# Kernel tuning notes

Hardware: AMD Instinct MI355X
Metric: run time of the kernel (lower is better)

The kernel has to match this reference:

```python
import jax, jax.numpy as jnp
import numpy as np

H = 16          # query heads
HKV = 4         # kv heads
DK = 128        # head_qk_dim
DV = 128        # head_v_dim
HID = 2048
KSZ = 4         # conv kernel size
EPS = 1e-5
NORMALIZER = 16.0


def _causal_dwconv_silu(x, w):
    # x: (B,S,C), w: (C,K). Causal depthwise conv then SiLU.
    B, S, C = x.shape
    K = w.shape[1]
    xp = jnp.pad(x, ((0, 0), (K - 1, 0), (0, 0)))
    y = jnp.zeros_like(x)
    for i in range(K):  # K=4, tiny fixed loop
        y = y + w[:, i] * xp[:, i:i + S, :]
    return jax.nn.silu(y)


def _l2norm(x, eps=1e-6):
    return x * jax.lax.rsqrt(jnp.sum(x * x, axis=-1, keepdims=True) + eps)


def setup_inputs() -> dict:
    key = jax.random.key(0)
    ks = jax.random.split(key, 8)
    B, S = 2, 2048
    qkv_dim = H * DK + HKV * DK + HKV * DV  # 3072
    s = lambda fan_in: 1.0 / np.sqrt(fan_in)
    return {
        "hidden_states": jax.random.normal(ks[0], (B, S, HID), jnp.float32),
        "qkv_w": jax.random.uniform(ks[1], (qkv_dim, HID), jnp.float32, -s(HID), s(HID)),
        "g_w": jax.random.uniform(ks[2], (H * DV, HID), jnp.float32, -s(HID), s(HID)),
        "b_w": jax.random.uniform(ks[3], (H, HID), jnp.float32, -s(HID), s(HID)),
        "gk_w": jax.random.uniform(ks[4], (H, HID), jnp.float32, -s(HID), s(HID)),
        "conv_w": jax.random.uniform(ks[5], (qkv_dim, KSZ), jnp.float32, -s(KSZ), s(KSZ)),
        "out_norm_w": jnp.ones((DV,), jnp.float32),
        "o_w": jax.random.uniform(ks[6], (HID, H * DV), jnp.float32, -s(H * DV), s(H * DV)),
    }


def reference(hidden_states, qkv_w, g_w, b_w, gk_w, conv_w, out_norm_w, o_w):
    x = hidden_states
    B, S, _ = x.shape
    grp = H // HKV

    qkv = x @ qkv_w.T                                   # (B,S,3072)
    qkv = _causal_dwconv_silu(qkv, conv_w)
    q, k, v = jnp.split(qkv, [H * DK, H * DK + HKV * DK], axis=-1)
    q = q.reshape(B, S, H, DK)
    k = k.reshape(B, S, HKV, DK)
    v = v.reshape(B, S, HKV, DV)
    # GQA expansion
    k = jnp.repeat(k, grp, axis=2)                      # (B,S,H,DK)
    v = jnp.repeat(v, grp, axis=2)                      # (B,S,H,DV)

    # q/k L2 norm + scale
    q = _l2norm(q) * (DK ** -0.5)
    k = _l2norm(k)

    # decay gate (logsigmoid, log-space), write strength beta
    g_log = jax.nn.log_sigmoid(x @ gk_w.T) / NORMALIZER  # (B,S,H)
    alpha = jnp.exp(g_log)
    beta = jax.nn.sigmoid(x @ b_w.T)                     # (B,S,H)

    # gated delta rule: S_t = a_t*S_{t-1} + k_t (x) beta_t*(v_t - k_t @ (a_t*S_{t-1}))
    def step(Sstate, inp):
        q_t, k_t, v_t, a_t, b_t = inp                    # (B,H,*)
        Sstate = Sstate * a_t[..., None, None]           # (B,H,DK,DV)
        v_pred = jnp.einsum('bhk,bhkv->bhv', k_t, Sstate)
        delta = (v_t - v_pred) * b_t[..., None]
        Sstate = Sstate + jnp.einsum('bhk,bhv->bhkv', k_t, delta)
        o_t = jnp.einsum('bhk,bhkv->bhv', q_t, Sstate)
        return Sstate, o_t

    tfirst = lambda a: jnp.moveaxis(a, 1, 0)             # (S,B,H,...)
    S0 = jnp.zeros((B, H, DK, DV), x.dtype)
    _, o = jax.lax.scan(step, S0, (tfirst(q), tfirst(k), tfirst(v), tfirst(alpha), tfirst(beta)))
    o = jnp.moveaxis(o, 0, 1)                            # (B,S,H,DV)

    # gated per-head RMSNorm then output projection
    g = (x @ g_w.T).reshape(B, S, H, DV)
    o = o * jax.lax.rsqrt(jnp.mean(o * o, axis=-1, keepdims=True) + EPS) * out_norm_w
    o = o * jax.nn.silu(g)
    return (o.reshape(B, S, H * DV)) @ o_w.T
```

## Files before the change

kernel.cpp:

```cpp
#include <hip/hip_runtime.h>
#include <math.h>

#define S_LEN 2048
#define BATCH 2
#define NH 16
#define NKV 4
#define DKQ 128
#define DVV 128
#define HID 2048
#define QKV_DIM 3072
#define M_TOK 4096

typedef _Float16 halfx8 __attribute__((ext_vector_type(8)));
typedef _Float16 halfx4 __attribute__((ext_vector_type(4)));
typedef float floatx4 __attribute__((ext_vector_type(4)));

#define AS1 __attribute__((address_space(1)))
#define AS3 __attribute__((address_space(3)))
#define GLD16(gp, lp) __builtin_amdgcn_global_load_lds((AS1 const void*)(gp), (AS3 void*)(lp), 16, 0, 0)
#define MFMA16(a, b, c) __builtin_amdgcn_mfma_f32_16x16x32_f16(a, b, c, 0, 0, 0)
#define SBAR() asm volatile("s_barrier" ::: "memory")

#define PA_STRIDE 81920

__device__ __forceinline__ float sigmoidf_(float x) { return 1.f / (1.f + __expf(-x)); }

__global__ __launch_bounds__(256) void cvt_f16(const float* __restrict__ in,
                                               _Float16* __restrict__ out, int n8) {
  int i = blockIdx.x * 256 + threadIdx.x;
  if (i >= n8) return;
  const float4* p = (const float4*)in;
  float4 a = p[2 * (size_t)i], b = p[2 * (size_t)i + 1];
  halfx8 o;
  o[0] = (_Float16)a.x; o[1] = (_Float16)a.y; o[2] = (_Float16)a.z; o[3] = (_Float16)a.w;
  o[4] = (_Float16)b.x; o[5] = (_Float16)b.y; o[6] = (_Float16)b.z; o[7] = (_Float16)b.w;
  *(halfx8*)(out + (size_t)i * 8) = o;
}

__global__ __launch_bounds__(256, 2) void gemm_bt_f16_2ph(const _Float16* __restrict__ A,
                                                          const _Float16* __restrict__ B,
                                                          float* __restrict__ C,
                                                          int M, int N, int K) {
  __shared__ char lds[65536] __attribute__((aligned(16)));
  const int tid = threadIdx.x;
  const int wid = tid >> 6, l = tid & 63;
  const int lr = l & 15, hi = l >> 4;
  const int wm = wid & 1, wn = wid >> 1;

  int nbx = gridDim.x;
  int bid = blockIdx.y * nbx + blockIdx.x;
  int nwg = nbx * gridDim.y;
  int swz = (nwg & 7) ? bid : ((bid & 7) * (nwg >> 3) + (bid >> 3));
  int bm = (swz / nbx) * 128, bn = (swz % nbx) * 128;

  const int srow = tid >> 3;
  const int csrc = ((tid & 7) ^ ((tid >> 3) & 7)) * 8;
  const _Float16* ga[4];
  const _Float16* gb[4];
#pragma unroll
  for (int q = 0; q < 4; ++q) {
    ga[q] = A + (size_t)(bm + q * 32 + srow) * K + csrc;
    gb[q] = B + (size_t)(bn + q * 32 + srow) * K + csrc;
  }
  const int dstA = tid * 16;
  const int dstB = 16384 + tid * 16;

  int cr[2];
  cr[0] = (hi ^ (lr & 7)) * 16;
  cr[1] = ((4 + hi) ^ (lr & 7)) * 16;
  const int abase = wm * 8192 + lr * 128;
  const int bbase = 16384 + wn * 8192 + lr * 128;

  floatx4 acc[4][4];
#pragma unroll
  for (int i = 0; i < 4; ++i)
#pragma unroll
    for (int j = 0; j < 4; ++j) acc[i][j] = (floatx4){0.f, 0.f, 0.f, 0.f};

  const int NT = K >> 6;
#define STAGE8(tt, pp)                                           \
  {                                                              \
    int kof = (tt) * 64;                                         \
    int pof = (pp) * 32768;                                      \
    _Pragma("unroll") for (int q = 0; q < 4; ++q) {              \
      GLD16(ga[q] + kof, lds + pof + q * 4096 + dstA);           \
      GLD16(gb[q] + kof, lds + pof + q * 4096 + dstB);           \
    }                                                            \
  }

  STAGE8(0, 0);
  asm volatile("s_waitcnt vmcnt(0)" ::: "memory");
  SBAR();

  halfx8 af[4][2], bf[2][2];
  for (int t = 0; t < NT; ++t) {
    const char* bufc = lds + (t & 1) * 32768;
    if (t + 1 < NT) STAGE8(t + 1, (t + 1) & 1);
#pragma unroll
    for (int mi = 0; mi < 4; ++mi)
#pragma unroll
      for (int ks = 0; ks < 2; ++ks)
        af[mi][ks] = *(const halfx8*)(bufc + abase + mi * 2048 + cr[ks]);
#pragma unroll
    for (int ni = 0; ni < 2; ++ni)
#pragma unroll
      for (int ks = 0; ks < 2; ++ks)
        bf[ni][ks] = *(const halfx8*)(bufc + bbase + ni * 2048 + cr[ks]);
    SBAR();
    __builtin_amdgcn_s_setprio(1);
#pragma unroll
    for (int mi = 0; mi < 4; ++mi)
#pragma unroll
      for (int ni = 0; ni < 2; ++ni)
#pragma unroll
        for (int ks = 0; ks < 2; ++ks)
          acc[mi][ni] = MFMA16(af[mi][ks], bf[ni][ks], acc[mi][ni]);
    __builtin_amdgcn_s_setprio(0);
    SBAR();
#pragma unroll
    for (int ni = 0; ni < 2; ++ni)
#pragma unroll
      for (int ks = 0; ks < 2; ++ks)
        bf[ni][ks] = *(const halfx8*)(bufc + bbase + (ni + 2) * 2048 + cr[ks]);
    SBAR();
    __builtin_amdgcn_s_setprio(1);
#pragma unroll
    for (int mi = 0; mi < 4; ++mi)
#pragma unroll
      for (int ni = 0; ni < 2; ++ni)
#pragma unroll
        for (int ks = 0; ks < 2; ++ks)
          acc[mi][ni + 2] = MFMA16(af[mi][ks], bf[ni][ks], acc[mi][ni + 2]);
    __builtin_amdgcn_s_setprio(0);
    asm volatile("s_waitcnt vmcnt(0)" ::: "memory");
    SBAR();
  }
#pragma unroll
  for (int mi = 0; mi < 4; ++mi)
#pragma unroll
    for (int ni = 0; ni < 4; ++ni) {
      int row0 = bm + wm * 64 + mi * 16 + hi * 4;
      int col = bn + wn * 64 + ni * 16 + lr;
#pragma unroll
      for (int r = 0; r < 4; ++r)
        C[(size_t)(row0 + r) * N + col] = acc[mi][ni][r];
    }
#undef STAGE8
}

__global__ __launch_bounds__(256) void gkb_kernel(const float* __restrict__ X,
                                                  const float* __restrict__ gk_w,
                                                  const float* __restrict__ b_w,
                                                  float* __restrict__ glog,
                                                  float* __restrict__ be) {
  __shared__ float xs[16][260];
  __shared__ float ws[32][260];
  int tid = threadIdx.x;
  int m0 = blockIdx.x * 16;
  int tl = tid >> 4, n0 = tid & 15;
  float acc0 = 0.f, acc1 = 0.f;
  for (int k0 = 0; k0 < HID; k0 += 256) {
#pragma unroll
    for (int i = 0; i < 4; ++i) {
      int F = i * 256 + tid;
      int r = F >> 6, c4 = (F & 63) * 4;
      *(float4*)&xs[r][c4] = *(const float4*)&X[(size_t)(m0 + r) * HID + k0 + c4];
    }
#pragma unroll
    for (int i = 0; i < 8; ++i) {
      int F = i * 256 + tid;
      int r = F >> 6, c4 = (F & 63) * 4;
      const float* src = (r < 16) ? (gk_w + (size_t)r * HID) : (b_w + (size_t)(r - 16) * HID);
      *(float4*)&ws[r][c4] = *(const float4*)&src[k0 + c4];
    }
    __syncthreads();
#pragma unroll 16
    for (int k = 0; k < 256; k += 4) {
      float4 a = *(const float4*)&xs[tl][k];
      float4 w0 = *(const float4*)&ws[n0][k];
      float4 w1 = *(const float4*)&ws[n0 + 16][k];
      acc0 += a.x * w0.x + a.y * w0.y + a.z * w0.z + a.w * w0.w;
      acc1 += a.x * w1.x + a.y * w1.y + a.z * w1.z + a.w * w1.w;
    }
    __syncthreads();
  }
  int m = m0 + tl, b = m >> 11, s = m & (S_LEN - 1);
  float z = acc0;
  float ls = (z >= 0.f) ? -log1pf(expf(-z)) : (z - log1pf(expf(z)));
  size_t oi = (size_t)(b * NH + n0) * S_LEN + s;
  glog[oi] = ls * 0.0625f;
  be[oi] = sigmoidf_(acc1);
}

__global__ __launch_bounds__(256) void conv_kernel(const float* __restrict__ qkv,
                                                   const float* __restrict__ conv_w,
                                                   float* __restrict__ qn,
                                                   float* __restrict__ kn,
                                                   float* __restrict__ vn) {
  __shared__ float ys[QKV_DIM];
  __shared__ float sc[20];
  int m = blockIdx.x;
  int b = m >> 11, s = m & (S_LEN - 1);
  int tid = threadIdx.x;
  for (int c = tid; c < QKV_DIM; c += 256) {
    float acc = 0.f;
#pragma unroll
    for (int i = 0; i < 4; ++i) {
      int si = s - 3 + i;
      if (si >= 0) acc += conv_w[c * 4 + i] * qkv[(size_t)(b * S_LEN + si) * QKV_DIM + c];
    }
    ys[c] = acc * (1.f / (1.f + __expf(-acc)));
  }
  __syncthreads();
  int wv = tid >> 6, lane = tid & 63;
  for (int ch = wv; ch < 20; ch += 4) {
    int base = (ch < 16) ? ch * 128 : 2048 + (ch - 16) * 128;
    float x0 = ys[base + lane], x1 = ys[base + 64 + lane];
    float ss = x0 * x0 + x1 * x1;
#pragma unroll
    for (int off = 1; off < 64; off <<= 1) ss += __shfl_xor(ss, off);
    float scale = rsqrtf(ss + 1e-6f);
    if (ch < 16) scale *= 0.08838834764831845f;
    if (lane == 0) sc[ch] = scale;
  }
  __syncthreads();
  for (int c = tid; c < 2048; c += 256) {
    int h = c >> 7, d = c & 127;
    qn[((size_t)(b * NH + h) * S_LEN + s) * DKQ + d] = ys[c] * sc[h];
  }
  for (int c = tid; c < 512; c += 256) {
    int j = c >> 7, d = c & 127;
    kn[((size_t)(b * NKV + j) * S_LEN + s) * DKQ + d] = ys[2048 + c] * sc[16 + j];
    vn[((size_t)(b * NKV + j) * S_LEN + s) * DVV + d] = ys[2560 + c];
  }
}

__global__ __launch_bounds__(256, 2) void phaseA_kernel(const float* __restrict__ qn,
                                                        const float* __restrict__ kn,
                                                        const float* __restrict__ vn,
                                                        const float* __restrict__ glog,
                                                        const float* __restrict__ be,
                                                        char* __restrict__ pout,
                                                        float* __restrict__ obuf) {
  __shared__ char smem[80128] __attribute__((aligned(16)));
  _Float16* kh = (_Float16*)smem;
  _Float16* qh = (_Float16*)(smem + 22528);
  float*    LT = (float*)(smem + 45056);
  _Float16* Ph = (_Float16*)(smem + 67584);
  float*    sc_c    = (float*)(smem + 78848);
  float*    sc_beta = sc_c + 64;
  float*    sc_gam  = sc_c + 128;
  float*    sc_bg   = sc_c + 192;
  float*    sc_gcr  = sc_c + 256;
  _Float16* Dt = (_Float16*)smem;
  _Float16* Wt = (_Float16*)(smem + 22528);
  _Float16* Kt = (_Float16*)(smem + 45056);

  int u = blockIdx.x;
  int bh = u >> 5, ch = u & 31;
  int t0 = ch * 64;
  int b = bh >> 4, h = bh & 15, kvh = h >> 2;
  const float* qb = qn + ((size_t)bh * S_LEN + t0) * DKQ;
  const float* kb = kn + (((size_t)(b * NKV + kvh)) * S_LEN + t0) * DKQ;
  const float* vb = vn + (((size_t)(b * NKV + kvh)) * S_LEN + t0) * DVV;
  const float* gl = glog + (size_t)bh * S_LEN + t0;
  const float* ber = be + (size_t)bh * S_LEN + t0;
  char* base = pout + (size_t)u * PA_STRIDE;
  _Float16* M_out = (_Float16*)base;
  _Float16* E_out = (_Float16*)(base + 32768);
  _Float16* B_out = (_Float16*)(base + 49152);
  float* ob = obuf + ((size_t)bh * S_LEN + t0) * DVV;

  int tid = threadIdx.x;
  if (tid < 64) {
    float x = gl[tid];
#pragma unroll
    for (int off = 1; off < 64; off <<= 1) {
      float y = __shfl_up(x, off);
      if (tid >= off) x += y;
    }
    sc_c[tid] = x;
  }
#pragma unroll
  for (int i = 0; i < 8; ++i) {
    int idx = i * 256 + tid;
    int t = idx >> 5, d4 = (idx & 31) * 4;
    float4 kv4 = *(const float4*)&kb[(size_t)t * DKQ + d4];
    float4 qv4 = *(const float4*)&qb[(size_t)t * DKQ + d4];
    _Float16* kd = &kh[t * 152 + d4];
    kd[0] = (_Float16)kv4.x; kd[1] = (_Float16)kv4.y; kd[2] = (_Float16)kv4.z; kd[3] = (_Float16)kv4.w;
    _Float16* qd = &qh[t * 152 + d4];
    qd[0] = (_Float16)qv4.x; qd[1] = (_Float16)qv4.y; qd[2] = (_Float16)qv4.z; qd[3] = (_Float16)qv4.w;
  }
  __syncthreads();
  if (tid < 64) {
    float c = sc_c[tid], c63 = sc_c[63];
    float gam = __expf(c);
    float bet = ber[tid];
    sc_gam[tid] = gam; sc_beta[tid] = bet; sc_bg[tid] = bet * gam;
    sc_gcr[tid] = __expf(c63 - c);
  }
  __syncthreads();

  float z[64];
  {
    const float* src = (tid < 128) ? vb : kb;
    const float* mult = (tid < 128) ? sc_beta : sc_bg;
    int col = tid & 127;
#pragma unroll
    for (int t = 0; t < 64; ++t) z[t] = mult[t] * src[(size_t)t * 128 + col];
  }

  int w = tid >> 6, l = tid & 63;
  int lr = l & 15, lk8 = (l >> 4) * 8, q4 = (l >> 4) * 4;
  floatx4 acc[8];
#pragma unroll
  for (int i = 0; i < 8; ++i) acc[i] = (floatx4){0.f, 0.f, 0.f, 0.f};
#pragma unroll
  for (int job = 0; job < 8; ++job) {
    int j2 = w * 8 + job;
    int tm = (j2 & 15) >> 2, tn = j2 & 3;
    const _Float16* Ar = (j2 < 16) ? kh : qh;
#pragma unroll
    for (int kk = 0; kk < 4; ++kk) {
      halfx8 af = *(const halfx8*)&Ar[(tm * 16 + lr) * 152 + kk * 32 + lk8];
      halfx8 bf = *(const halfx8*)&kh[(tn * 16 + lr) * 152 + kk * 32 + lk8];
      acc[job] = MFMA16(af, bf, acc[job]);
    }
  }
#pragma unroll
  for (int job = 0; job < 8; ++job) {
    int j2 = w * 8 + job;
    int tm = (j2 & 15) >> 2, tn = j2 & 3;
    int jcol = tn * 16 + lr;
    float cj = sc_c[jcol];
#pragma unroll
    for (int r = 0; r < 4; ++r) {
      int trow = tm * 16 + q4 + r;
      float val = acc[job][r] * __expf(sc_c[trow] - cj);
      if (j2 < 16) {
        LT[jcol * 68 + trow] = (jcol < trow) ? sc_beta[trow] * val : 0.f;
      } else {
        Ph[trow * 88 + jcol] = (_Float16)((jcol <= trow) ? val : 0.f);
      }
    }
  }
  __syncthreads();

#pragma unroll
  for (int t = 0; t < 64; ++t) {
    float zt = z[t];
    const int start = ((t + 1) >> 2) << 2;
#pragma unroll
    for (int t2 = start; t2 < 64; t2 += 4) {
      float4 lv = *(const float4*)&LT[t * 68 + t2];
      z[t2 + 0] -= lv.x * zt;
      z[t2 + 1] -= lv.y * zt;
      z[t2 + 2] -= lv.z * zt;
      z[t2 + 3] -= lv.w * zt;
    }
  }
  floatx4 Eacc[8];
#pragma unroll
  for (int ni = 0; ni < 8; ++ni)
#pragma unroll
    for (int r = 0; r < 4; ++r) {
      int trow = w * 16 + q4 + r;
      Eacc[ni][r] = sc_gam[trow] * (float)qh[trow * 152 + ni * 16 + lr];
    }
  __syncthreads();

  {
    int d = tid >> 1, tb = (tid & 1) * 32;
#pragma unroll
    for (int j = 0; j < 4; ++j) {
      halfx8 kv;
#pragma unroll
      for (int r = 0; r < 8; ++r) {
        int t = tb + j * 8 + r;
        kv[r] = (_Float16)(sc_gcr[t] * (float)kh[t * 152 + d]);
      }
      *(halfx8*)&Kt[d * 88 + tb + j * 8] = kv;
    }
  }
  if (tid >= 128) {
    int col = tid & 127;
#pragma unroll
    for (int t = 0; t < 64; t += 8) {
      halfx8 wv;
#pragma unroll
      for (int r = 0; r < 8; ++r) wv[r] = (_Float16)(-z[t + r]);
      *(halfx8*)&Wt[col * 88 + t] = wv;
    }
  }
  __syncthreads();
  if (tid < 128) {
    int col = tid & 127;
#pragma unroll
    for (int t = 0; t < 64; t += 8) {
      halfx8 dv;
#pragma unroll
      for (int r = 0; r < 8; ++r) dv[r] = (_Float16)z[t + r];
      *(halfx8*)&Dt[col * 88 + t] = dv;
    }
  }
  __syncthreads();

  floatx4 Macc[2][8], Bacc[2][8], Oacc[8];
  float gC = __expf(sc_c[63]);
#pragma unroll
  for (int mi = 0; mi < 2; ++mi)
#pragma unroll
    for (int ni = 0; ni < 8; ++ni) {
#pragma unroll
      for (int r = 0; r < 4; ++r)
        Macc[mi][ni][r] = ((w * 32 + mi * 16 + q4 + r) == (ni * 16 + lr)) ? gC : 0.f;
      Bacc[mi][ni] = (floatx4){0.f, 0.f, 0.f, 0.f};
    }
#pragma unroll
  for (int ni = 0; ni < 8; ++ni) Oacc[ni] = (floatx4){0.f, 0.f, 0.f, 0.f};
#pragma unroll
  for (int ks = 0; ks < 2; ++ks) {
    halfx8 ka0 = *(const halfx8*)&Kt[(w * 32 + lr) * 88 + ks * 32 + lk8];
    halfx8 ka1 = *(const halfx8*)&Kt[(w * 32 + 16 + lr) * 88 + ks * 32 + lk8];
    halfx8 pa = *(const halfx8*)&Ph[(w * 16 + lr) * 88 + ks * 32 + lk8];
#pragma unroll
    for (int ni = 0; ni < 8; ++ni) {
      halfx8 wb = *(const halfx8*)&Wt[(ni * 16 + lr) * 88 + ks * 32 + lk8];
      halfx8 db = *(const halfx8*)&Dt[(ni * 16 + lr) * 88 + ks * 32 + lk8];
      Macc[0][ni] = MFMA16(ka0, wb, Macc[0][ni]);
      Macc[1][ni] = MFMA16(ka1, wb, Macc[1][ni]);
      Bacc[0][ni] = MFMA16(ka0, db, Bacc[0][ni]);
      Bacc[1][ni] = MFMA16(ka1, db, Bacc[1][ni]);
      Eacc[ni] = MFMA16(pa, wb, Eacc[ni]);
      Oacc[ni] = MFMA16(pa, db, Oacc[ni]);
    }
  }
#pragma unroll
  for (int mi = 0; mi < 2; ++mi)
#pragma unroll
    for (int ni = 0; ni < 8; ++ni)
#pragma unroll
      for (int r = 0; r < 4; ++r) {
        int row = w * 32 + mi * 16 + q4 + r;
        M_out[row * 128 + ni * 16 + lr] = (_Float16)Macc[mi][ni][r];
        B_out[ni * 2048 + row * 16 + lr] = (_Float16)Bacc[mi][ni][r];
      }
#pragma unroll
  for (int ni = 0; ni < 8; ++ni)
#pragma unroll
    for (int r = 0; r < 4; ++r) {
      int trow = w * 16 + q4 + r;
      E_out[trow * 128 + ni * 16 + lr] = (_Float16)Eacc[ni][r];
      ob[(size_t)trow * 128 + ni * 16 + lr] = Oacc[ni][r];
    }
}

__global__ __launch_bounds__(256, 1) void phaseB_kernel(const char* __restrict__ pin,
                                                        float* __restrict__ obuf) {
  __shared__ _Float16 Mh[2][128 * 152];
  __shared__ _Float16 Eh[2][64 * 152];
  __shared__ _Float16 St[2][16 * 152];

  int bh = blockIdx.x & 31, vg = blockIdx.x >> 5;
  int tid = threadIdx.x, w = tid >> 6, l = tid & 63;
  int lr = l & 15, lk8 = (l >> 4) * 8, q4 = (l >> 4) * 4;
  const char* ub0 = pin + (size_t)(bh * 32) * PA_STRIDE;
  float* ob_base = obuf + (size_t)bh * S_LEN * DVV + vg * 16;

  float4 Mr[8], Er[4];
  float Bc[2][4], Oc[4], Bn[2][4], On[4];

  {
    const float4* Mg = (const float4*)ub0;
    const float4* Eg = (const float4*)(ub0 + 32768);
    const _Float16* Bg = (const _Float16*)(ub0 + 49152) + vg * 2048;
#pragma unroll
    for (int j = 0; j < 8; ++j) Mr[j] = Mg[j * 256 + tid];
#pragma unroll
    for (int j = 0; j < 4; ++j) Er[j] = Eg[j * 256 + tid];
#pragma unroll
    for (int mi = 0; mi < 2; ++mi)
#pragma unroll
      for (int r = 0; r < 4; ++r)
        Bc[mi][r] = (float)Bg[(w * 32 + mi * 16 + q4 + r) * 16 + lr];
#pragma unroll
    for (int r = 0; r < 4; ++r)
      Oc[r] = ob_base[(size_t)(w * 16 + q4 + r) * DVV + lr];
#pragma unroll
    for (int j = 0; j < 8; ++j) {
      int n = j * 256 + tid;
      *(float4*)&Mh[0][(n >> 4) * 152 + (n & 15) * 8] = Mr[j];
    }
#pragma unroll
    for (int j = 0; j < 4; ++j) {
      int n = j * 256 + tid;
      *(float4*)&Eh[0][(n >> 4) * 152 + (n & 15) * 8] = Er[j];
    }
    halfx4 z4;
    z4[0] = (_Float16)0.f; z4[1] = (_Float16)0.f; z4[2] = (_Float16)0.f; z4[3] = (_Float16)0.f;
#pragma unroll
    for (int mi = 0; mi < 2; ++mi)
      *(halfx4*)&St[0][lr * 152 + w * 32 + mi * 16 + q4] = z4;
  }
  asm volatile("s_waitcnt lgkmcnt(0)" ::: "memory");

  for (int c = 0; c < 32; ++c) {
    __builtin_amdgcn_s_barrier();
    int cur = c & 1, nxt = cur ^ 1;
    bool have = (c + 1) < 32;
    if (have) {
      const char* un = ub0 + (size_t)(c + 1) * PA_STRIDE;
      const float4* Mg = (const float4*)un;
      const float4* Eg = (const float4*)(un + 32768);
      const _Float16* Bg = (const _Float16*)(un + 49152) + vg * 2048;
#pragma unroll
      for (int j = 0; j < 8; ++j) Mr[j] = Mg[j * 256 + tid];
#pragma unroll
      for (int j = 0; j < 4; ++j) Er[j] = Eg[j * 256 + tid];
#pragma unroll
      for (int mi = 0; mi < 2; ++mi)
#pragma unroll
        for (int r = 0; r < 4; ++r)
          Bn[mi][r] = (float)Bg[(w * 32 + mi * 16 + q4 + r) * 16 + lr];
#pragma unroll
      for (int r = 0; r < 4; ++r)
        On[r] = ob_base[(size_t)((c + 1) * 64 + w * 16 + q4 + r) * DVV + lr];
    }
    floatx4 Sn0 = {Bc[0][0], Bc[0][1], Bc[0][2], Bc[0][3]};
    floatx4 Sn1 = {Bc[1][0], Bc[1][1], Bc[1][2], Bc[1][3]};
    floatx4 Oa = {Oc[0], Oc[1], Oc[2], Oc[3]};
#pragma unroll
    for (int ks = 0; ks < 4; ++ks) {
      halfx8 sf = *(const halfx8*)&St[cur][lr * 152 + ks * 32 + lk8];
      halfx8 ma0 = *(const halfx8*)&Mh[cur][(w * 32 + lr) * 152 + ks * 32 + lk8];
      halfx8 ma1 = *(const halfx8*)&Mh[cur][(w * 32 + 16 + lr) * 152 + ks * 32 + lk8];
      halfx8 ea = *(const halfx8*)&Eh[cur][(w * 16 + lr) * 152 + ks * 32 + lk8];
      Sn0 = MFMA16(ma0, sf, Sn0);
      Sn1 = MFMA16(ma1, sf, Sn1);
      Oa = MFMA16(ea, sf, Oa);
    }
    {
      float* obr = ob_base + (size_t)c * 64 * DVV;
#pragma unroll
      for (int r = 0; r < 4; ++r)
        obr[(size_t)(w * 16 + q4 + r) * DVV + lr] = Oa[r];
    }
#pragma unroll
    for (int mi = 0; mi < 2; ++mi) {
      halfx4 sv;
      floatx4 Sm = mi ? Sn1 : Sn0;
#pragma unroll
      for (int r = 0; r < 4; ++r) sv[r] = (_Float16)Sm[r];
      *(halfx4*)&St[nxt][lr * 152 + w * 32 + mi * 16 + q4] = sv;
    }
    if (have) {
#pragma unroll
      for (int j = 0; j < 8; ++j) {
        int n = j * 256 + tid;
        *(float4*)&Mh[nxt][(n >> 4) * 152 + (n & 15) * 8] = Mr[j];
      }
#pragma unroll
      for (int j = 0; j < 4; ++j) {
        int n = j * 256 + tid;
        *(float4*)&Eh[nxt][(n >> 4) * 152 + (n & 15) * 8] = Er[j];
      }
#pragma unroll
      for (int mi = 0; mi < 2; ++mi)
#pragma unroll
        for (int r = 0; r < 4; ++r) Bc[mi][r] = Bn[mi][r];
#pragma unroll
      for (int r = 0; r < 4; ++r) Oc[r] = On[r];
    }
    asm volatile("s_waitcnt lgkmcnt(0)" ::: "memory");
  }
}

__global__ __launch_bounds__(256) void normgate_kernel(const float* __restrict__ o_buf,
                                                       const float* __restrict__ g_buf,
                                                       const float* __restrict__ nw,
                                                       _Float16* __restrict__ og) {
  int gid = blockIdx.x * 4 + (threadIdx.x >> 6);
  int lane = threadIdx.x & 63;
  int m = gid >> 4, h = gid & 15;
  int b = m >> 11, s = m & (S_LEN - 1);
  const float* orow = o_buf + ((size_t)(b * NH + h) * S_LEN + s) * DVV;
  float o0 = orow[lane], o1 = orow[lane + 64];
  float ss = o0 * o0 + o1 * o1;
#pragma unroll
  for (int off = 1; off < 64; off <<= 1) ss += __shfl_xor(ss, off);
  float r = rsqrtf(ss * (1.f / 128.f) + 1e-5f);
  size_t gi = (size_t)m * HID + h * DVV;
  float g0 = g_buf[gi + lane], g1 = g_buf[gi + lane + 64];
  og[gi + lane] = (_Float16)(o0 * r * nw[lane] * (g0 * sigmoidf_(g0)));
  og[gi + lane + 64] = (_Float16)(o1 * r * nw[lane + 64] * (g1 * sigmoidf_(g1)));
}

extern "C" void kernel_launch(void* const* d_in, const int* in_sizes, int n_in,
                              void* d_out, int out_size, void* d_ws, size_t ws_size,
                              hipStream_t stream) {
  const float* X      = (const float*)d_in[0];
  const float* qkv_w  = (const float*)d_in[1];
  const float* g_w    = (const float*)d_in[2];
  const float* b_w    = (const float*)d_in[3];
  const float* gk_w   = (const float*)d_in[4];
  const float* conv_w = (const float*)d_in[5];
  const float* norm_w = (const float*)d_in[6];
  const float* o_w    = (const float*)d_in[7];
  float* out = (float*)d_out;

  char* ws = (char*)d_ws;
  float* qkv_buf   = (float*)(ws);
  float* g_buf     = (float*)(ws);
  _Float16* ow16   = (_Float16*)(ws + 33554432);
  float* glog      = (float*)(ws + 41943040);
  float* be        = (float*)(ws + 42205184);
  float* qn        = (float*)(ws + 50331648);
  float* kn        = (float*)(ws + 83886080);
  float* vn        = (float*)(ws + 92274688);
  _Float16* X16    = (_Float16*)(ws + 100663296);
  _Float16* qw16   = (_Float16*)(ws + 117440512);
  _Float16* gw16   = (_Float16*)(ws + 130023424);
  char*  pA        = (char*)(ws + 100663296);
  _Float16* og16   = (_Float16*)(ws + 100663296);
  float* o_buf     = qn;

  dim3 blk(256);
  cvt_f16<<<dim3(4096), blk, 0, stream>>>(X, X16, 1048576);
  cvt_f16<<<dim3(3072), blk, 0, stream>>>(qkv_w, qw16, 786432);
  cvt_f16<<<dim3(2048), blk, 0, stream>>>(g_w, gw16, 524288);
  gemm_bt_f16_2ph<<<dim3(QKV_DIM / 128, M_TOK / 128), blk, 0, stream>>>(X16, qw16, qkv_buf, M_TOK, QKV_DIM, HID);
  conv_kernel<<<dim3(M_TOK), blk, 0, stream>>>(qkv_buf, conv_w, qn, kn, vn);
  gkb_kernel<<<dim3(M_TOK / 16), blk, 0, stream>>>(X, gk_w, b_w, glog, be);
  cvt_f16<<<dim3(2048), blk, 0, stream>>>(o_w, ow16, 524288);
  gemm_bt_f16_2ph<<<dim3(HID / 128, M_TOK / 128), blk, 0, stream>>>(X16, gw16, g_buf, M_TOK, HID, HID);
  phaseA_kernel<<<dim3(1024), blk, 0, stream>>>(qn, kn, vn, glog, be, pA, o_buf);
  phaseB_kernel<<<dim3(256), blk, 0, stream>>>(pA, o_buf);
  normgate_kernel<<<dim3(M_TOK * NH / 4), blk, 0, stream>>>(o_buf, g_buf, norm_w, og16);
  gemm_bt_f16_2ph<<<dim3(HID / 128, M_TOK / 128), blk, 0, stream>>>(og16, ow16, out, M_TOK, HID, HID);
}
```

Baseline: 487.8 us.

## Restructure conv kernel to slide a register window over 8 tokens per wave

The causal depthwise conv kernel now gives each wave 8 consecutive tokens of one 128-channel head slot. It keeps the previous three inputs in registers as a sliding window, so each qkv element is read from global memory once per wave instead of four times. The per-head L2 norm becomes a wave shuffle reduction with no shared memory or block barriers. The grid changes from one block per token to a 2D tile×slot launch, and the conv weights are loaded once as float4 per thread.

```diff
diff --git a/kernel.cpp b/kernel.cpp
--- a/kernel.cpp
+++ b/kernel.cpp
@@ -197,41 +197,52 @@
                                                    float* __restrict__ qn,
                                                    float* __restrict__ kn,
                                                    float* __restrict__ vn) {
-  __shared__ float ys[QKV_DIM];
-  __shared__ float sc[20];
-  int m = blockIdx.x;
-  int b = m >> 11, s = m & (S_LEN - 1);
-  int tid = threadIdx.x;
-  for (int c = tid; c < QKV_DIM; c += 256) {
-    float acc = 0.f;
-#pragma unroll
-    for (int i = 0; i < 4; ++i) {
-      int si = s - 3 + i;
-      if (si >= 0) acc += conv_w[c * 4 + i] * qkv[(size_t)(b * S_LEN + si) * QKV_DIM + c];
-    }
-    ys[c] = acc * (1.f / (1.f + __expf(-acc)));
-  }
-  __syncthreads();
-  int wv = tid >> 6, lane = tid & 63;
-  for (int ch = wv; ch < 20; ch += 4) {
-    int base = (ch < 16) ? ch * 128 : 2048 + (ch - 16) * 128;
-    float x0 = ys[base + lane], x1 = ys[base + 64 + lane];
-    float ss = x0 * x0 + x1 * x1;
-#pragma unroll
-    for (int off = 1; off < 64; off <<= 1) ss += __shfl_xor(ss, off);
-    float scale = rsqrtf(ss + 1e-6f);
-    if (ch < 16) scale *= 0.08838834764831845f;
-    if (lane == 0) sc[ch] = scale;
-  }
-  __syncthreads();
-  for (int c = tid; c < 2048; c += 256) {
-    int h = c >> 7, d = c & 127;
-    qn[((size_t)(b * NH + h) * S_LEN + s) * DKQ + d] = ys[c] * sc[h];
-  }
-  for (int c = tid; c < 512; c += 256) {
-    int j = c >> 7, d = c & 127;
-    kn[((size_t)(b * NKV + j) * S_LEN + s) * DKQ + d] = ys[2048 + c] * sc[16 + j];
-    vn[((size_t)(b * NKV + j) * S_LEN + s) * DVV + d] = ys[2560 + c];
+  int tile = blockIdx.x, slot = blockIdx.y;
+  int w = threadIdx.x >> 6, l = threadIdx.x & 63;
+  int m0 = tile * 32 + w * 8;
+  int b = m0 >> 11, s0 = m0 & (S_LEN - 1);
+  int cbase = (slot < 16) ? slot * 128 : (slot < 20 ? 2048 + (slot - 16) * 128
+                                                    : 2560 + (slot - 20) * 128);
+  int c0 = cbase + l, c1 = c0 + 64;
+  float4 wv0 = *(const float4*)&conv_w[c0 * 4];
+  float4 wv1 = *(const float4*)&conv_w[c1 * 4];
+
+  float a0[3], a1[3];
+#pragma unroll
+  for (int i = 0; i < 3; ++i) {
+    int si = s0 - 3 + i;
+    bool v = si >= 0;
+    const float* rp = qkv + (size_t)(m0 - 3 + i) * QKV_DIM;
+    a0[i] = v ? rp[c0] : 0.f;
+    a1[i] = v ? rp[c1] : 0.f;
+  }
+
+  float* outp;
+  if (slot < 16)      outp = qn + ((size_t)(b * NH + slot) * S_LEN + s0) * DKQ;
+  else if (slot < 20) outp = kn + ((size_t)(b * NKV + (slot - 16)) * S_LEN + s0) * DKQ;
+  else                outp = vn + ((size_t)(b * NKV + (slot - 20)) * S_LEN + s0) * DVV;
+
+#pragma unroll
+  for (int j = 0; j < 8; ++j) {
+    const float* rp = qkv + (size_t)(m0 + j) * QKV_DIM;
+    float cur0 = rp[c0], cur1 = rp[c1];
+    float acc0 = wv0.x * a0[0] + wv0.y * a0[1] + wv0.z * a0[2] + wv0.w * cur0;
+    float acc1 = wv1.x * a1[0] + wv1.y * a1[1] + wv1.z * a1[2] + wv1.w * cur1;
+    float y0 = acc0 * (1.f / (1.f + __expf(-acc0)));
+    float y1 = acc1 * (1.f / (1.f + __expf(-acc1)));
+    if (slot < 20) {
+      float ss = y0 * y0 + y1 * y1;
+#pragma unroll
+      for (int off = 1; off < 64; off <<= 1) ss += __shfl_xor(ss, off);
+      float scale = rsqrtf(ss + 1e-6f);
+      if (slot < 16) scale *= 0.08838834764831845f;
+      y0 *= scale;
+      y1 *= scale;
+    }
+    outp[(size_t)j * 128 + l] = y0;
+    outp[(size_t)j * 128 + l + 64] = y1;
+    a0[0] = a0[1]; a0[1] = a0[2]; a0[2] = cur0;
+    a1[0] = a1[1]; a1[1] = a1[2]; a1[2] = cur1;
   }
 }
 
@@ -630,7 +641,7 @@
   cvt_f16<<<dim3(3072), blk, 0, stream>>>(qkv_w, qw16, 786432);
   cvt_f16<<<dim3(2048), blk, 0, stream>>>(g_w, gw16, 524288);
   gemm_bt_f16_2ph<<<dim3(QKV_DIM / 128, M_TOK / 128), blk, 0, stream>>>(X16, qw16, qkv_buf, M_TOK, QKV_DIM, HID);
-  conv_kernel<<<dim3(M_TOK), blk, 0, stream>>>(qkv_buf, conv_w, qn, kn, vn);
+  conv_kernel<<<dim3(M_TOK / 32, 24), blk, 0, stream>>>(qkv_buf, conv_w, qn, kn, vn);
   gkb_kernel<<<dim3(M_TOK / 16), blk, 0, stream>>>(X, gk_w, b_w, glog, be);
   cvt_f16<<<dim3(2048), blk, 0, stream>>>(o_w, ow16, 524288);
   gemm_bt_f16_2ph<<<dim3(HID / 128, M_TOK / 128), blk, 0, stream>>>(X16, gw16, g_buf, M_TOK, HID, HID);
```

Measured after the change: 434.4 us. -10.9%, faster.
